# Optimization experiments

Hardware: AMD Instinct MI355X
Metric: run time of the kernel (lower is better)

Reference implementation:

```python
import jax, jax.numpy as jnp
import numpy as np

BANDS, ROWS, SIM_THRESH = 16, 8, 0.5


def setup_inputs() -> dict:
    key = jax.random.key(0)
    k1, k2 = jax.random.split(key)
    N, D = 8192, 256
    Z = jax.random.normal(k1, (N, D), dtype=jnp.float32)
    # random hyperplanes ~ N(0, I), (bands*rows, D) -- sampled once (torch samples in forward)
    planes = jax.random.normal(k2, (BANDS * ROWS, D), dtype=jnp.float32)
    return {"Z": Z, "planes": planes}


def reference(Z, planes):
    N, D = Z.shape
    # signature: sign of projections, (bands, rows, N); +/-1 vs bool is equivalent for bucketing
    sig_bits = (planes @ Z.T >= 0).reshape(BANDS, ROWS, N)
    # bit-pack each band's row-signature into an integer key == hashing the signature bytes
    bit_weights = (2 ** jnp.arange(ROWS)).astype(jnp.int32)
    keys = jnp.einsum('brn,r->bn', sig_bits.astype(jnp.int32), bit_weights)  # (bands, N)
    # cosine pairwise similarity (row-normalized GEMM)
    Zn = Z / jnp.linalg.norm(Z, axis=1, keepdims=True)
    sim = Zn @ Zn.T  # (N, N)
    # number of bands in which i and j fall in the same LSH bucket
    def band_match(acc, k):
        return acc + (k[:, None] == k[None, :]).astype(jnp.float32), None
    counts, _ = jax.lax.scan(band_match, jnp.zeros((N, N), jnp.float32), keys)
    # original masks the diagonal with -inf, thresholds at sim_thresh, and emits one
    # (sim) entry per matching band into an uncoalesced sparse tensor; densified this
    # is counts * sim on surviving off-diagonal pairs.
    mask = (sim >= SIM_THRESH) & (~jnp.eye(N, dtype=bool))
    return jnp.where(mask, counts * sim, 0.0)
```

## Files before the change

kernel.cpp:

```cpp
#include <hip/hip_runtime.h>

typedef __attribute__((ext_vector_type(4))) float floatx4;

#define N_PTS 8192
#define D_DIM 256
#define N_PLANES 128
#define NTILE 64

__device__ inline int zbytes(unsigned int w) {
    unsigned int t = ((w & 0x7f7f7f7fu) + 0x7f7f7f7fu) | w | 0x7f7f7f7fu;
    return __popc(~t);
}

__device__ inline void load_lds16(const void* g, void* l) {
    __builtin_amdgcn_global_load_lds(
        (const __attribute__((address_space(1))) unsigned int*)g,
        (__attribute__((address_space(3))) unsigned int*)l, 16, 0, 0);
}

__global__ void norm_kernel(const float* __restrict__ Z,
                            unsigned char* __restrict__ Zn) {
    int n = blockIdx.x;
    int lane = threadIdx.x;
    const float4* zr = (const float4*)(Z + (size_t)n * D_DIM);
    float4 v = zr[lane];
    float ss = v.x * v.x + v.y * v.y + v.z * v.z + v.w * v.w;
#pragma unroll
    for (int off = 32; off > 0; off >>= 1) ss += __shfl_down(ss, off);
    ss = __shfl(ss, 0);
    float inv = rsqrtf(ss);
    int p = __builtin_amdgcn_cvt_pk_fp8_f32(v.x * inv, v.y * inv, 0, false);
    p = __builtin_amdgcn_cvt_pk_fp8_f32(v.z * inv, v.w * inv, p, true);
    ((int*)(Zn + (size_t)n * D_DIM))[lane] = p;
}

__global__ __launch_bounds__(256) void keys_kernel(
    const float* __restrict__ Z, const float* __restrict__ planes,
    unsigned int* __restrict__ keys4) {
    __shared__ __align__(16) float zs[16][D_DIM];
    int t = threadIdx.x;
    int base = blockIdx.x * 16;

    const float4* zsrc = (const float4*)(Z + (size_t)base * D_DIM);
    float4* zdst = (float4*)&zs[0][0];
#pragma unroll
    for (int i = 0; i < 4; ++i) zdst[t + i * 256] = zsrc[t + i * 256];
    __syncthreads();

    int p = t & 127;
    int hf = t >> 7;
    int wave = t >> 6, lane = t & 63;
    const float4* pr = (const float4*)(planes + (size_t)p * D_DIM);

    float acc[8] = {};
    for (int kk = 0; kk < D_DIM / 4; ++kk) {
        float4 pv = pr[kk];
#pragma unroll
        for (int j = 0; j < 8; ++j) {
            float4 zv = *(const float4*)&zs[hf * 8 + j][kk * 4];
            acc[j] += pv.x * zv.x + pv.y * zv.y + pv.z * zv.z + pv.w * zv.w;
        }
    }

#pragma unroll
    for (int j = 0; j < 8; ++j) {
        unsigned long long mask = __ballot(acc[j] >= 0.0f);
        if (lane < 2) {
            keys4[(size_t)(base + hf * 8 + j) * 4 + (wave & 1) * 2 + lane] =
                (unsigned int)(mask >> (32 * lane));
        }
    }
}

__global__ __launch_bounds__(256, 4) void gemm_kernel(
    const unsigned char* __restrict__ Zn, const uint4* __restrict__ keys,
    float* __restrict__ out) {
    __shared__ __align__(16) unsigned char As[8192];
    __shared__ __align__(16) unsigned char Bs[8192];
    __shared__ uint4 krow[128];
    __shared__ uint4 kcol[128];

    int idx = blockIdx.x;
    int bi = (int)((129.0f - sqrtf(16641.0f - 8.0f * (float)idx)) * 0.5f);
    while ((bi + 1) * NTILE - ((bi + 1) * bi) / 2 <= idx) ++bi;
    while (bi * NTILE - (bi * (bi - 1)) / 2 > idx) --bi;
    int bj = bi + (idx - (bi * NTILE - (bi * (bi - 1)) / 2));
    int rowBase = bi * 128;
    int colBase = bj * 128;
    bool diag = (bi == bj);

    int t = threadIdx.x;
    if (t < 128)
        krow[t] = keys[rowBase + t];
    else
        kcol[t - 128] = keys[colBase + (t - 128)];

    const unsigned char* ZnA = Zn + (size_t)rowBase * D_DIM;
    const unsigned char* ZnB = Zn + (size_t)colBase * D_DIM;

    int wave = t >> 6, lane = t & 63;
    int wm = wave >> 1, wn = wave & 1;
    int quad = lane >> 4, l16 = lane & 15;

    floatx4 acc[4][4] = {};

    for (int s = 0; s < 4; ++s) {
        __syncthreads();
#pragma unroll
        for (int i = 0; i < 2; ++i) {
            int sa = i * 256 + t;
            int c = sa >> 7, row = sa & 127;
            size_t gOff = (size_t)row * D_DIM + s * 64 + c * 16;
            load_lds16(ZnA + gOff, &As[sa * 16]);
            load_lds16(ZnB + gOff, &Bs[sa * 16]);
        }
        __syncthreads();

#pragma unroll
        for (int k2 = 0; k2 < 2; ++k2) {
            int kByte = k2 * 32 + quad * 8;
            int cc = kByte >> 4;
            int off8 = kByte & 8;
            long afr[4], bfr[4];
#pragma unroll
            for (int mt = 0; mt < 4; ++mt)
                afr[mt] = *(const long*)&As[(cc * 128 + wm * 64 + mt * 16 + l16) * 16 + off8];
#pragma unroll
            for (int nt = 0; nt < 4; ++nt)
                bfr[nt] = *(const long*)&Bs[(cc * 128 + wn * 64 + nt * 16 + l16) * 16 + off8];
#pragma unroll
            for (int mt = 0; mt < 4; ++mt)
#pragma unroll
                for (int nt = 0; nt < 4; ++nt)
                    acc[mt][nt] = __builtin_amdgcn_mfma_f32_16x16x32_fp8_fp8(
                        afr[mt], bfr[nt], acc[mt][nt], 0, 0, 0);
        }
    }

    {
        floatx4 z4 = {0.f, 0.f, 0.f, 0.f};
        float* ownQ = out + (size_t)(rowBase + wm * 64 + quad * 16) * N_PTS +
                      colBase + wn * 64 + l16 * 4;
        float* mirQ = out + (size_t)(colBase + wn * 64 + quad * 16) * N_PTS +
                      rowBase + wm * 64 + l16 * 4;
#pragma unroll
        for (int i = 0; i < 16; ++i)
            __builtin_nontemporal_store(z4, (floatx4*)(ownQ + (size_t)i * N_PTS));
        if (!diag) {
#pragma unroll
            for (int i = 0; i < 16; ++i)
                __builtin_nontemporal_store(z4, (floatx4*)(mirQ + (size_t)i * N_PTS));
        }
    }

    bool any = false;
#pragma unroll
    for (int mt = 0; mt < 4; ++mt)
#pragma unroll
        for (int nt = 0; nt < 4; ++nt)
#pragma unroll
            for (int r = 0; r < 4; ++r) {
                int gi = rowBase + wm * 64 + mt * 16 + quad * 4 + r;
                int gj = colBase + wn * 64 + nt * 16 + l16;
                any = any || (acc[mt][nt][r] >= 0.5f && gi != gj);
            }

    if (__ballot(any)) {
        __builtin_amdgcn_s_waitcnt(0x0f70);
#pragma unroll
        for (int mt = 0; mt < 4; ++mt)
#pragma unroll
            for (int nt = 0; nt < 4; ++nt) {
                int lj = wn * 64 + nt * 16 + l16;
                int gj = colBase + lj;
                uint4 kj = kcol[lj];
#pragma unroll
                for (int r = 0; r < 4; ++r) {
                    int liL = wm * 64 + mt * 16 + quad * 4 + r;
                    int gi = rowBase + liL;
                    float s = acc[mt][nt][r];
                    if (s >= 0.5f && gi != gj) {
                        uint4 ki = krow[liL];
                        int c = zbytes(ki.x ^ kj.x) + zbytes(ki.y ^ kj.y) +
                                zbytes(ki.z ^ kj.z) + zbytes(ki.w ^ kj.w);
                        float v = s * (float)c;
                        out[(size_t)gi * N_PTS + gj] = v;
                        if (!diag) out[(size_t)gj * N_PTS + gi] = v;
                    }
                }
            }
    }
}

extern "C" void kernel_launch(void* const* d_in, const int* in_sizes, int n_in,
                              void* d_out, int out_size, void* d_ws,
                              size_t ws_size, hipStream_t stream) {
    const float* Z = (const float*)d_in[0];
    const float* planes = (const float*)d_in[1];
    float* out = (float*)d_out;

    unsigned char* Zn = (unsigned char*)d_ws;
    unsigned int* keys4 =
        (unsigned int*)((char*)d_ws + (size_t)N_PTS * D_DIM);

    norm_kernel<<<N_PTS, 64, 0, stream>>>(Z, Zn);
    keys_kernel<<<N_PTS / 16, 256, 0, stream>>>(Z, planes, keys4);
    int nblocks = NTILE * (NTILE + 1) / 2;
    gemm_kernel<<<nblocks, 256, 0, stream>>>(Zn, (const uint4*)keys4, out);
}
```

Before: 304.0 us.

## Fuse normalization into keys kernel, widen GEMM K-stage, overlap zero stores with loads

Folds the per-row normalization and FP8 quantization into the keys kernel, reusing the Z rows already staged in shared memory, which removes one kernel launch and a second read of Z. The GEMM now loads K in two stages of 128 bytes instead of four of 64, doubling the LDS buffers to cut barrier count. It also issues the output zero-fill stores for the tile's own block during the second load stage, so they overlap the global-to-LDS copy. The larger LDS footprint may reduce occupancy, and the earlier stores add memory traffic during compute.

```diff
diff --git a/kernel.cpp b/kernel.cpp
--- a/kernel.cpp
+++ b/kernel.cpp
@@ -18,25 +18,9 @@
         (__attribute__((address_space(3))) unsigned int*)l, 16, 0, 0);
 }
 
-__global__ void norm_kernel(const float* __restrict__ Z,
-                            unsigned char* __restrict__ Zn) {
-    int n = blockIdx.x;
-    int lane = threadIdx.x;
-    const float4* zr = (const float4*)(Z + (size_t)n * D_DIM);
-    float4 v = zr[lane];
-    float ss = v.x * v.x + v.y * v.y + v.z * v.z + v.w * v.w;
-#pragma unroll
-    for (int off = 32; off > 0; off >>= 1) ss += __shfl_down(ss, off);
-    ss = __shfl(ss, 0);
-    float inv = rsqrtf(ss);
-    int p = __builtin_amdgcn_cvt_pk_fp8_f32(v.x * inv, v.y * inv, 0, false);
-    p = __builtin_amdgcn_cvt_pk_fp8_f32(v.z * inv, v.w * inv, p, true);
-    ((int*)(Zn + (size_t)n * D_DIM))[lane] = p;
-}
-
-__global__ __launch_bounds__(256) void keys_kernel(
+__global__ __launch_bounds__(256) void keys_norm_kernel(
     const float* __restrict__ Z, const float* __restrict__ planes,
-    unsigned int* __restrict__ keys4) {
+    unsigned int* __restrict__ keys4, unsigned char* __restrict__ Zn) {
     __shared__ __align__(16) float zs[16][D_DIM];
     int t = threadIdx.x;
     int base = blockIdx.x * 16;
@@ -46,6 +30,27 @@
 #pragma unroll
     for (int i = 0; i < 4; ++i) zdst[t + i * 256] = zsrc[t + i * 256];
     __syncthreads();
+
+    {
+        int row = t >> 4, ch = t & 15;
+        const float* zr = &zs[row][ch * 16];
+        float ss = 0.f;
+#pragma unroll
+        for (int i = 0; i < 16; ++i) ss += zr[i] * zr[i];
+#pragma unroll
+        for (int off = 8; off > 0; off >>= 1) ss += __shfl_xor(ss, off);
+        float inv = rsqrtf(ss);
+        int4 o;
+#pragma unroll
+        for (int q = 0; q < 4; ++q) {
+            int p = __builtin_amdgcn_cvt_pk_fp8_f32(zr[q * 4] * inv,
+                                                    zr[q * 4 + 1] * inv, 0, false);
+            p = __builtin_amdgcn_cvt_pk_fp8_f32(zr[q * 4 + 2] * inv,
+                                                zr[q * 4 + 3] * inv, p, true);
+            ((int*)&o)[q] = p;
+        }
+        *(int4*)(Zn + (size_t)(base + row) * D_DIM + ch * 16) = o;
+    }
 
     int p = t & 127;
     int hf = t >> 7;
@@ -75,8 +80,8 @@
 __global__ __launch_bounds__(256, 4) void gemm_kernel(
     const unsigned char* __restrict__ Zn, const uint4* __restrict__ keys,
     float* __restrict__ out) {
-    __shared__ __align__(16) unsigned char As[8192];
-    __shared__ __align__(16) unsigned char Bs[8192];
+    __shared__ __align__(16) unsigned char As[16384];
+    __shared__ __align__(16) unsigned char Bs[16384];
     __shared__ uint4 krow[128];
     __shared__ uint4 kcol[128];
 
@@ -102,22 +107,33 @@
     int wm = wave >> 1, wn = wave & 1;
     int quad = lane >> 4, l16 = lane & 15;
 
+    float* ownQ = out + (size_t)(rowBase + wm * 64 + quad * 16) * N_PTS +
+                  colBase + wn * 64 + l16 * 4;
+    float* mirQ = out + (size_t)(colBase + wn * 64 + quad * 16) * N_PTS +
+                  rowBase + wm * 64 + l16 * 4;
+    floatx4 z4 = {0.f, 0.f, 0.f, 0.f};
+
     floatx4 acc[4][4] = {};
 
-    for (int s = 0; s < 4; ++s) {
+    for (int s = 0; s < 2; ++s) {
         __syncthreads();
 #pragma unroll
-        for (int i = 0; i < 2; ++i) {
+        for (int i = 0; i < 4; ++i) {
             int sa = i * 256 + t;
             int c = sa >> 7, row = sa & 127;
-            size_t gOff = (size_t)row * D_DIM + s * 64 + c * 16;
+            size_t gOff = (size_t)row * D_DIM + s * 128 + c * 16;
             load_lds16(ZnA + gOff, &As[sa * 16]);
             load_lds16(ZnB + gOff, &Bs[sa * 16]);
         }
+        if (s == 1) {
+#pragma unroll
+            for (int i = 0; i < 16; ++i)
+                __builtin_nontemporal_store(z4, (floatx4*)(ownQ + (size_t)i * N_PTS));
+        }
         __syncthreads();
 
 #pragma unroll
-        for (int k2 = 0; k2 < 2; ++k2) {
+        for (int k2 = 0; k2 < 4; ++k2) {
             int kByte = k2 * 32 + quad * 8;
             int cc = kByte >> 4;
             int off8 = kByte & 8;
@@ -137,20 +153,10 @@
         }
     }
 
-    {
-        floatx4 z4 = {0.f, 0.f, 0.f, 0.f};
-        float* ownQ = out + (size_t)(rowBase + wm * 64 + quad * 16) * N_PTS +
-                      colBase + wn * 64 + l16 * 4;
-        float* mirQ = out + (size_t)(colBase + wn * 64 + quad * 16) * N_PTS +
-                      rowBase + wm * 64 + l16 * 4;
+    if (!diag) {
 #pragma unroll
         for (int i = 0; i < 16; ++i)
-            __builtin_nontemporal_store(z4, (floatx4*)(ownQ + (size_t)i * N_PTS));
-        if (!diag) {
-#pragma unroll
-            for (int i = 0; i < 16; ++i)
-                __builtin_nontemporal_store(z4, (floatx4*)(mirQ + (size_t)i * N_PTS));
-        }
+            __builtin_nontemporal_store(z4, (floatx4*)(mirQ + (size_t)i * N_PTS));
     }
 
     bool any = false;
@@ -203,8 +209,7 @@
     unsigned int* keys4 =
         (unsigned int*)((char*)d_ws + (size_t)N_PTS * D_DIM);
 
-    norm_kernel<<<N_PTS, 64, 0, stream>>>(Z, Zn);
-    keys_kernel<<<N_PTS / 16, 256, 0, stream>>>(Z, planes, keys4);
+    keys_norm_kernel<<<N_PTS / 16, 256, 0, stream>>>(Z, planes, keys4, Zn);
     int nblocks = NTILE * (NTILE + 1) / 2;
     gemm_kernel<<<nblocks, 256, 0, stream>>>(Zn, (const uint4*)keys4, out);
 }
```

Result: no change. 299.5 us (-1.5%).
